# Performance work log

Hardware: AMD Instinct MI355X
Metric: run time of the kernel (lower is better)

## Reference

```python
import jax, jax.numpy as jnp
import numpy as np

DIM = 4096; H = 32; D = 128; EPS = 1e-5
BLOCK = 16
BD = 8; MAXB = 64                    # decode seqs, blocks per decode seq
PB = 2; PSEQ = 1024; TP = PB * PSEQ  # prefill: 2 seqs x 1024 tokens
TOK = TP + BD
NBLOCKS = BD * MAXB + TP // BLOCK    # 640
NEG = -1e30


def setup_inputs() -> dict:
    key = jax.random.key(0)
    ks = jax.random.split(key, 10)
    std = 0.02
    x = jax.random.normal(ks[0], (TOK, DIM), jnp.float32)
    key_heap = jax.random.normal(ks[1], (NBLOCKS, BLOCK, H, D), jnp.float32)
    val_heap = jax.random.normal(ks[2], (NBLOCKS, BLOCK, H, D), jnp.float32)
    # decode seq i owns blocks [i*MAXB, (i+1)*MAXB); context_len includes the new token
    ctx = jax.random.randint(ks[3], (BD,), 256, MAXB * BLOCK + 1).astype(jnp.int32)
    block_table = (jnp.arange(BD)[:, None] * MAXB + jnp.arange(MAXB)[None, :]).astype(jnp.int32)
    prefill_slots = BD * MAXB * BLOCK + jnp.arange(TP)      # prefill fills blocks after decode region
    decode_slots = jnp.arange(BD) * MAXB * BLOCK + (ctx - 1)  # newest-token slot per decode seq
    slot_mapping = jnp.concatenate([prefill_slots, decode_slots]).astype(jnp.int32)
    cu = (jnp.arange(PB + 1) * PSEQ).astype(jnp.int32)
    return dict(
        x=x, key_heap=key_heap, val_heap=val_heap,
        slot_mapping=slot_mapping, decode_block_table=block_table,
        decode_context_lens=ctx, prefill_cu_seqlens=cu,
        num_prefill_tokens=TP, prefill_max_seqlen=PSEQ, decode_max_seq_len=MAXB * BLOCK,
        norm1_w=1.0 + std * jax.random.normal(ks[4], (DIM,), jnp.float32),
        norm2_w=1.0 + std * jax.random.normal(ks[5], (DIM,), jnp.float32),
        w_qkv_w=std * jax.random.normal(ks[6], (3 * H * D, DIM), jnp.float32),
        wo_w=std * jax.random.normal(ks[7], (DIM, H * D), jnp.float32),
        w_gate_up_w=std * jax.random.normal(ks[8], (8 * DIM, DIM), jnp.float32),
        w2_w=std * jax.random.normal(ks[9], (DIM, 4 * DIM), jnp.float32),
    )


def _rmsnorm(x, w):
    return x * jax.lax.rsqrt(jnp.mean(x * x, -1, keepdims=True) + EPS) * w


def _forward(x, key_heap, val_heap, norm1_w, norm2_w, w_qkv_w, wo_w, w_gate_up_w, w2_w,
             slot_mapping, decode_block_table, decode_context_lens, prefill_cu_seqlens,
             num_prefill_tokens):
    T = x.shape[0]
    scale = 1.0 / np.sqrt(D)
    residual = x
    # fused norm1 -> QKV projection
    qkv = (_rmsnorm(x, norm1_w) @ w_qkv_w.T).reshape(T, 3, H, D)
    q, k, v = qkv[:, 0], qkv[:, 1], qkv[:, 2]
    # paged cache write (ops.reshape_and_cache)
    nb, bs = key_heap.shape[0], key_heap.shape[1]
    key_flat = key_heap.reshape(nb * bs, H, D).at[slot_mapping].set(k)
    val_flat = val_heap.reshape(nb * bs, H, D).at[slot_mapping].set(v)
    # prefill: varlen causal self-attention (flash_attn_varlen_func)
    Tp = num_prefill_tokens
    pos = jnp.arange(Tp)
    seg = jnp.searchsorted(prefill_cu_seqlens, pos, side='right') - 1
    mask = (seg[:, None] == seg[None, :]) & (pos[:, None] >= pos[None, :])  # [Tp,Tp]
    s = jnp.einsum('ihd,jhd->hij', q[:Tp], k[:Tp]) * scale
    attn_p = jnp.einsum('hij,jhd->ihd',
                        jax.nn.softmax(jnp.where(mask[None], s, NEG), -1), v[:Tp])
    # decode: paged attention over cached KV (ops.paged_attention_v2)
    kd = key_flat.reshape(nb, bs, H, D)[decode_block_table].reshape(BD, -1, H, D)
    vd = val_flat.reshape(nb, bs, H, D)[decode_block_table].reshape(BD, -1, H, D)
    L = kd.shape[1]
    sd = jnp.einsum('bhd,blhd->bhl', q[Tp:], kd) * scale
    dmask = jnp.arange(L)[None, :] < decode_context_lens[:, None]
    attn_d = jnp.einsum('bhl,blhd->bhd',
                        jax.nn.softmax(jnp.where(dmask[:, None, :], sd, NEG), -1), vd)
    attn = jnp.concatenate([attn_p.reshape(Tp, H * D), attn_d.reshape(BD, H * D)], 0)
    # MLP: wo + residual, norm2, SwiGLU, down-proj, residual
    h = attn @ wo_w.T + residual
    residual = h
    gu = _rmsnorm(h, norm2_w) @ w_gate_up_w.T
    g, u = jnp.split(gu, 2, -1)
    return (jax.nn.silu(g) * u) @ w2_w.T + residual


def reference(x, key_heap, val_heap, slot_mapping, decode_block_table, decode_context_lens,
              prefill_cu_seqlens, num_prefill_tokens, prefill_max_seqlen, decode_max_seq_len,
              norm1_w, norm2_w, w_qkv_w, wo_w, w_gate_up_w, w2_w):
    del prefill_max_seqlen, decode_max_seq_len  # kernel scheduling hints only
    return _forward(x, key_heap, val_heap, norm1_w, norm2_w, w_qkv_w, wo_w, w_gate_up_w, w2_w,
                    slot_mapping, decode_block_table, decode_context_lens, prefill_cu_seqlens,
                    num_prefill_tokens)
```

## Files before the change

### kernel.cpp

```cpp
#include <hip/hip_runtime.h>
#include <hip/hip_bf16.h>
#include <stdint.h>

#define DIMC   4096
#define HC     32
#define DC     128
#define TPC    2048
#define TOKC   2056
#define BDC    8
#define MAXBC  64
#define PSEQC  1024
#define QKVN   12288
#define FFNC   16384
#define PSCALE 0.08838834764831843f

typedef __attribute__((ext_vector_type(8))) short short8;
typedef __attribute__((ext_vector_type(4))) float f32x4;
typedef __attribute__((ext_vector_type(4))) unsigned short u16x4;
typedef __attribute__((ext_vector_type(8))) unsigned short u16x8;

__device__ inline unsigned short f2bf(float f) {
  union { float f; unsigned u; } v; v.f = f;
  unsigned r = v.u + 0x7FFFu + ((v.u >> 16) & 1u);
  return (unsigned short)(r >> 16);
}
__device__ inline float bf2f(unsigned short u) {
  union { unsigned u; float f; } v; v.u = ((unsigned)u) << 16;
  return v.f;
}
__device__ inline f32x4 mfma16(short8 a, short8 b, f32x4 c) {
  return __builtin_amdgcn_mfma_f32_16x16x32_bf16(a, b, c, 0, 0, 0);
}
__device__ inline void gload16(const void* g, void* l) {
  __builtin_amdgcn_global_load_lds(
      (const __attribute__((address_space(1))) void*)g,
      (__attribute__((address_space(3))) void*)l, 16, 0, 0);
}

__global__ __launch_bounds__(256) void cvt_w(
    const float* __restrict__ in, unsigned short* __restrict__ out, long n8)
{
  long i = (long)blockIdx.x * 256 + threadIdx.x;
  const long stride = (long)gridDim.x * 256;
  for (; i < n8; i += stride) {
    f32x4 a = ((const f32x4*)in)[2 * i];
    f32x4 b = ((const f32x4*)in)[2 * i + 1];
    u16x8 o;
#pragma unroll
    for (int j = 0; j < 4; ++j) { o[j] = f2bf(a[j]); o[j + 4] = f2bf(b[j]); }
    ((u16x8*)out)[i] = o;
  }
}

__global__ __launch_bounds__(256) void rmsnorm_k(
    const float* __restrict__ x, const float* __restrict__ w,
    unsigned short* __restrict__ out)
{
  const int row = blockIdx.x;
  const int tid = threadIdx.x;
  const f32x4* xr = (const f32x4*)(x + (size_t)row * DIMC);
  f32x4 v[4];
  float ss = 0.f;
#pragma unroll
  for (int i = 0; i < 4; ++i) {
    v[i] = xr[i * 256 + tid];
    ss += v[i][0]*v[i][0] + v[i][1]*v[i][1] + v[i][2]*v[i][2] + v[i][3]*v[i][3];
  }
  for (int off = 32; off; off >>= 1) ss += __shfl_xor(ss, off);
  __shared__ float sred[4];
  if ((tid & 63) == 0) sred[tid >> 6] = ss;
  __syncthreads();
  const float rms = rsqrtf((sred[0]+sred[1]+sred[2]+sred[3]) * (1.f/DIMC) + 1e-5f);
  const f32x4* wr = (const f32x4*)w;
#pragma unroll
  for (int i = 0; i < 4; ++i) {
    f32x4 wv = wr[i * 256 + tid];
    u16x4 o;
#pragma unroll
    for (int j = 0; j < 4; ++j) o[j] = f2bf(v[i][j] * rms * wv[j]);
    *(u16x4*)(out + (size_t)row * DIMC + (size_t)(i * 256 + tid) * 4) = o;
  }
}

template<int MODE, int SK>
__global__ __launch_bounds__(512, 2) void gemm8p(
    const unsigned short* __restrict__ A, const unsigned short* __restrict__ Bh,
    float* __restrict__ Cf, unsigned short* __restrict__ Cb,
    const float* __restrict__ Res, int M, int N, int K)
{
  __shared__ char ldsc[131072];
  const int tid = threadIdx.x;
  const int lane = tid & 63, wid = tid >> 6;
  const int wr = wid >> 2, wc = wid & 3;
  const int lhi = lane >> 4, llo = lane & 15;

  const int nM = (M + 255) >> 8;
  const int nN = N >> 8;
  const int nwg = gridDim.x, orig = blockIdx.x;
  const int qq = nwg >> 3, rr = nwg & 7;
  const int xcd = orig & 7, lid = orig >> 3;
  const int wgid = (xcd < rr ? xcd*(qq+1) : rr*(qq+1) + (xcd-rr)*qq) + lid;
  const int tiles = nM * nN;
  const int ks = wgid / tiles;
  const int tile = wgid % tiles;
  const int bm = (tile % nM) << 8;
  const int bn = (tile / nM) << 8;
  const int kLen = K / SK;
  const int k0 = ks * kLen;
  const int NT = kLen >> 6;

  const unsigned short* src[2][2][2];
#pragma unroll
  for (int i = 0; i < 2; ++i) {
    int s = i * 512 + tid;
    int row = s >> 3;
    int chunk = (s & 7) ^ (row & 7);
#pragma unroll
    for (int h = 0; h < 2; ++h) {
      int ga = bm + h * 128 + row; ga = ga < M ? ga : M - 1;
      src[0][h][i] = A  + (size_t)ga * K + k0 + chunk * 8;
      src[1][h][i] = Bh + (size_t)(bn + h * 128 + row) * K + k0 + chunk * 8;
    }
  }

#define STG(U, OP, H) do { \
    int bb_ = (((U) & 1) << 16) + ((OP) << 15) + ((H) << 14) + (wid << 10); \
    gload16(src[OP][H][0] + ((size_t)(U) << 6), ldsc + bb_); \
    gload16(src[OP][H][1] + ((size_t)(U) << 6), ldsc + bb_ + 8192); \
  } while (0)

#define LDA(PB, HA) do { _Pragma("unroll") for (int m_ = 0; m_ < 4; ++m_) { \
    int row_ = wr*64 + m_*16 + llo; \
    int rb_ = (PB) + ((HA) << 14) + row_*128; int sx_ = (row_ & 7) << 4; \
    ar[m_][0] = *(const short8*)(ldsc + rb_ + ((lhi*16) ^ sx_)); \
    ar[m_][1] = *(const short8*)(ldsc + rb_ + ((64 + lhi*16) ^ sx_)); } } while (0)

#define LDB(PB, HB, DST) do { _Pragma("unroll") for (int n_ = 0; n_ < 2; ++n_) { \
    int row_ = wc*32 + n_*16 + llo; \
    int rb_ = (PB) + 32768 + ((HB) << 14) + row_*128; int sx_ = (row_ & 7) << 4; \
    DST[n_][0] = *(const short8*)(ldsc + rb_ + ((lhi*16) ^ sx_)); \
    DST[n_][1] = *(const short8*)(ldsc + rb_ + ((64 + lhi*16) ^ sx_)); } } while (0)

#define MM(QA, QB, B_) do { __builtin_amdgcn_s_setprio(1); \
    _Pragma("unroll") for (int m_ = 0; m_ < 4; ++m_) \
    _Pragma("unroll") for (int n_ = 0; n_ < 2; ++n_) { \
      acc[QA][QB][m_][n_] = mfma16(ar[m_][0], B_[n_][0], acc[QA][QB][m_][n_]); \
      acc[QA][QB][m_][n_] = mfma16(ar[m_][1], B_[n_][1], acc[QA][QB][m_][n_]); } \
    __builtin_amdgcn_s_setprio(0); } while (0)

#define FEN __builtin_amdgcn_sched_barrier(0)
#define BAR __builtin_amdgcn_s_barrier()
#define VMB(N) do { FEN; asm volatile("s_waitcnt vmcnt(" #N ")" ::: "memory"); \
    BAR; FEN; } while (0)

  f32x4 acc[2][2][4][2] = {};
  short8 ar[4][2], b0[2][2], b1[2][2];

  STG(0, 0, 0); STG(0, 1, 0); STG(0, 1, 1); STG(0, 0, 1);
  STG(1, 0, 0); STG(1, 1, 0); STG(1, 1, 1);
  VMB(6);
  LDA(0, 0); LDB(0, 0, b0);

  for (int t = 0; t < NT - 2; ++t) {
    const int pb = (t & 1) << 16, pbn = ((t + 1) & 1) << 16;
    LDB(pb, 1, b1);
    STG(t + 1, 0, 1);
    MM(0, 0, b0);
    BAR;
    STG(t + 2, 0, 0);
    MM(0, 1, b1);
    LDA(pb, 1);
    BAR;
    STG(t + 2, 1, 0);
    MM(1, 1, b1);
    VMB(8);
    STG(t + 2, 1, 1);
    MM(1, 0, b0);
    LDA(pbn, 0);
    LDB(pbn, 0, b0);
    VMB(6);
  }
  {
    const int pb = ((NT - 2) & 1) << 16, pbn = ((NT - 1) & 1) << 16;
    LDB(pb, 1, b1);
    STG(NT - 1, 0, 1);
    MM(0, 0, b0);
    BAR;
    MM(0, 1, b1);
    LDA(pb, 1);
    BAR;
    MM(1, 1, b1);
    VMB(4);
    MM(1, 0, b0);
    LDA(pbn, 0);
    LDB(pbn, 0, b0);
    VMB(0);
  }
  {
    const int pb = ((NT - 1) & 1) << 16;
    LDB(pb, 1, b1);
    MM(0, 0, b0);
    MM(0, 1, b1);
    LDA(pb, 1);
    MM(1, 1, b1);
    MM(1, 0, b0);
  }

  float* Pf = (MODE == 3) ? (Cf + (size_t)ks * M * N) : Cf;
#pragma unroll
  for (int qa = 0; qa < 2; ++qa)
#pragma unroll
  for (int m_ = 0; m_ < 4; ++m_)
#pragma unroll
  for (int j = 0; j < 4; ++j) {
    int row = bm + qa*128 + wr*64 + m_*16 + lhi*4 + j;
    if (row < M) {
#pragma unroll
      for (int qb = 0; qb < 2; ++qb)
#pragma unroll
      for (int n_ = 0; n_ < 2; ++n_) {
        int col = bn + qb*128 + wc*32 + n_*16 + llo;
        float v = acc[qa][qb][m_][n_][j];
        if (MODE == 1) { v += Res[(size_t)row*N + col]; Pf[(size_t)row*N + col] = v; }
        else if (MODE == 3) { Pf[(size_t)row*N + col] = v; }
        else Cb[(size_t)row*N + col] = f2bf(v);
      }
    }
  }
#undef STG
#undef LDA
#undef LDB
#undef MM
#undef FEN
#undef BAR
#undef VMB
}

__global__ __launch_bounds__(256) void redk(
    const float* __restrict__ p, const float* __restrict__ res,
    float* __restrict__ out, long n4)
{
  long i = (long)blockIdx.x * 256 + threadIdx.x;
  if (i >= n4) return;
  const f32x4* p4 = (const f32x4*)p;
  f32x4 v = p4[i] + p4[i + n4] + p4[i + 2*n4] + p4[i + 3*n4]
          + ((const f32x4*)res)[i];
  ((f32x4*)out)[i] = v;
}

template<int MODE, int BF16B>
__global__ __launch_bounds__(256) void gemm_bt(
    const unsigned short* __restrict__ A, const float* __restrict__ Bf,
    const unsigned short* __restrict__ Bh,
    float* __restrict__ Cf, unsigned short* __restrict__ Cb,
    const float* __restrict__ Res, int M, int N, int K)
{
  __shared__ unsigned short la[128 * 64];
  __shared__ unsigned short lb[128 * 64];
  const int tid = threadIdx.x;
  const int lane = tid & 63, wid = tid >> 6;
  const int wr = wid >> 1, wc = wid & 1;
  const int lhi = lane >> 4, llo = lane & 15;

  const int nM = (M + 127) >> 7;
  const int nwg = gridDim.x;
  const int orig = blockIdx.x;
  const int qq = nwg >> 3, rr = nwg & 7;
  const int xcd = orig & 7, lid = orig >> 3;
  const int wgid = (xcd < rr ? xcd * (qq + 1) : rr * (qq + 1) + (xcd - rr) * qq) + lid;
  const int bm = (wgid % nM) * 128;
  const int bn = (wgid / nM) * 128;

  const unsigned short* aSrc[4];
  const unsigned short* bSrcH[4];
  char* aDst[4];
  char* bDst[4];
#pragma unroll
  for (int p = 0; p < 4; ++p) {
    int slot = p * 256 + tid;
    int row = slot >> 3;
    int chunk = (slot & 7) ^ (row & 7);
    int gr = bm + row; gr = gr < M ? gr : M - 1;
    aSrc[p] = A + (size_t)gr * K + chunk * 8;
    aDst[p] = (char*)la + p * 4096 + wid * 1024;
    if (BF16B) {
      bSrcH[p] = Bh + (size_t)(bn + row) * K + chunk * 8;
      bDst[p] = (char*)lb + p * 4096 + wid * 1024;
    }
  }

  f32x4 acc[4][4] = {};

  for (int k0 = 0; k0 < K; k0 += 64) {
#pragma unroll
    for (int p = 0; p < 4; ++p) gload16(aSrc[p] + k0, aDst[p]);
    if (BF16B) {
#pragma unroll
      for (int p = 0; p < 4; ++p) gload16(bSrcH[p] + k0, bDst[p]);
    } else {
#pragma unroll
      for (int p = 0; p < 4; ++p) {
        int idx = p * 256 + tid;
        int row = idx >> 3, c8 = (idx & 7) << 3;
        const float* srcf = Bf + (size_t)(bn + row) * K + k0 + c8;
        f32x4 v0 = *(const f32x4*)srcf;
        f32x4 v1 = *(const f32x4*)(srcf + 4);
        short8 bv;
#pragma unroll
        for (int i = 0; i < 4; ++i) { bv[i] = (short)f2bf(v0[i]); bv[i+4] = (short)f2bf(v1[i]); }
        int byt = (row << 7) + (c8 << 1);
        byt ^= (row & 7) << 4;
        *(short8*)((char*)lb + byt) = bv;
      }
    }
    __syncthreads();
#pragma unroll
    for (int kk = 0; kk < 64; kk += 32) {
      short8 af[4], bfr[4];
#pragma unroll
      for (int m = 0; m < 4; ++m) {
        int row = wr * 64 + m * 16 + llo;
        int byt = (row << 7) + ((kk + lhi * 8) << 1);
        byt ^= (row & 7) << 4;
        af[m] = *(const short8*)((const char*)la + byt);
      }
#pragma unroll
      for (int n = 0; n < 4; ++n) {
        int row = wc * 64 + n * 16 + llo;
        int byt = (row << 7) + ((kk + lhi * 8) << 1);
        byt ^= (row & 7) << 4;
        bfr[n] = *(const short8*)((const char*)lb + byt);
      }
#pragma unroll
      for (int m = 0; m < 4; ++m)
#pragma unroll
        for (int n = 0; n < 4; ++n)
          acc[m][n] = mfma16(af[m], bfr[n], acc[m][n]);
    }
    __syncthreads();
  }

#pragma unroll
  for (int m = 0; m < 4; ++m) {
#pragma unroll
    for (int j = 0; j < 4; ++j) {
      int row = bm + wr * 64 + m * 16 + lhi * 4 + j;
      if (row < M) {
#pragma unroll
        for (int n = 0; n < 4; ++n) {
          int col = bn + wc * 64 + n * 16 + llo;
          float v = acc[m][n][j];
          if (MODE == 1) {
            v += Res[(size_t)row * N + col];
            Cf[(size_t)row * N + col] = v;
          } else {
            Cb[(size_t)row * N + col] = f2bf(v);
          }
        }
      }
    }
  }
}

__global__ __launch_bounds__(512) void prefill_attn(
    const unsigned short* __restrict__ qkv, unsigned short* __restrict__ attnb)
{
  const int h = blockIdx.x, qtb = blockIdx.y, s = blockIdx.z;
  const int seq0 = s * PSEQC;
  const int q0 = qtb * 128;
  const int tid = threadIdx.x;
  const int lane = tid & 63, w = tid >> 6;
  const int lhi = lane >> 4, llo = lane & 15;
  const int qw = q0 + w * 16;

  __shared__ unsigned short lk[64 * 128];
  __shared__ unsigned short lvt[128 * 72];
  __shared__ unsigned short lp[8][16 * 72];

  short8 qf[4];
  {
    const unsigned short* qrow =
        qkv + (size_t)(seq0 + qw + llo) * QKVN + h * DC;
#pragma unroll
    for (int kk = 0; kk < 4; ++kk)
      qf[kk] = *(const short8*)(qrow + kk * 32 + lhi * 8);
  }

  float m_r[4], l_r[4];
#pragma unroll
  for (int r = 0; r < 4; ++r) { m_r[r] = -1e30f; l_r[r] = 0.f; }
  f32x4 oacc[8] = {};

  const int ntiles = 2 * qtb + 2;
  for (int t = 0; t < ntiles; ++t) {
    const int j0 = t * 64;
#pragma unroll
    for (int p = 0; p < 2; ++p) {
      int idx = p * 512 + tid;
      int row = idx >> 4, cs = idx & 15;
      int cg = cs ^ (row & 7);
      gload16(qkv + (size_t)(seq0 + j0 + row) * QKVN + DIMC + h * DC + cg * 8,
              (char*)lk + p * 8192 + w * 1024);
    }
    {
      int jp = tid >> 4;
      int c8 = (tid & 15) << 3;
      int j = jp * 2;
      const unsigned short* vrow =
          qkv + (size_t)(seq0 + j0 + j) * QKVN + 2 * DIMC + h * DC + c8;
      short8 v0 = *(const short8*)vrow;
      short8 v1 = *(const short8*)(vrow + QKVN);
#pragma unroll
      for (int i = 0; i < 8; ++i) {
        int d = c8 + i;
        int jj = j ^ (((d >> 3) & 7) << 3);
        unsigned pack = (unsigned)(unsigned short)v0[i]
                      | ((unsigned)(unsigned short)v1[i] << 16);
        *(unsigned*)(lvt + d * 72 + jj) = pack;
      }
    }
    asm volatile("s_waitcnt vmcnt(0)" ::: "memory");
    __syncthreads();

    const bool active = (j0 <= qw + 15);
    if (active) {
      f32x4 sfr[4] = {};
#pragma unroll
      for (int n = 0; n < 4; ++n) {
        int row = n * 16 + llo;
#pragma unroll
        for (int kk = 0; kk < 4; ++kk) {
          int col = (kk * 32 + lhi * 8) ^ ((row & 7) << 3);
          short8 kf = *(const short8*)(lk + row * 128 + col);
          sfr[n] = mfma16(qf[kk], kf, sfr[n]);
        }
      }

      const bool diag = (j0 + 63 > qw);
      const int qbase = qw + lhi * 4;
      float pv[4][4];
#pragma unroll
      for (int r = 0; r < 4; ++r) {
        float mx = -1e30f;
#pragma unroll
        for (int n = 0; n < 4; ++n) {
          float sv = sfr[n][r] * PSCALE;
          if (diag && (j0 + n * 16 + llo > qbase + r)) sv = -1e30f;
          pv[n][r] = sv;
          mx = fmaxf(mx, sv);
        }
        for (int off = 8; off; off >>= 1) mx = fmaxf(mx, __shfl_xor(mx, off));
        float mnew = fmaxf(m_r[r], mx);
        float alpha = __expf(m_r[r] - mnew);
        m_r[r] = mnew;
        float rs = 0.f;
#pragma unroll
        for (int n = 0; n < 4; ++n) {
          float p = __expf(pv[n][r] - mnew);
          pv[n][r] = p;
          rs += p;
        }
        for (int off = 8; off; off >>= 1) rs += __shfl_xor(rs, off);
        l_r[r] = l_r[r] * alpha + rs;
#pragma unroll
        for (int f = 0; f < 8; ++f) oacc[f][r] *= alpha;
      }

      unsigned short* lpw = lp[w];
#pragma unroll
      for (int r = 0; r < 4; ++r)
#pragma unroll
        for (int n = 0; n < 4; ++n)
          lpw[(lhi * 4 + r) * 72 + n * 16 + llo] = f2bf(pv[n][r]);

#pragma unroll
      for (int kk = 0; kk < 2; ++kk) {
        short8 pf = *(const short8*)(lpw + llo * 72 + kk * 32 + lhi * 8);
#pragma unroll
        for (int f = 0; f < 8; ++f) {
          int d = f * 16 + llo;
          int jb = kk * 32 + lhi * 8;
          int jj = jb ^ (((d >> 3) & 7) << 3);
          short8 vf = *(const short8*)(lvt + d * 72 + jj);
          oacc[f] = mfma16(pf, vf, oacc[f]);
        }
      }
    }
    __syncthreads();
  }

#pragma unroll
  for (int r = 0; r < 4; ++r) {
    int row = seq0 + qw + lhi * 4 + r;
    float inv = 1.f / l_r[r];
#pragma unroll
    for (int f = 0; f < 8; ++f)
      attnb[(size_t)row * DIMC + h * DC + f * 16 + llo] = f2bf(oacc[f][r] * inv);
  }
}

__global__ __launch_bounds__(256) void decode_attn(
    const unsigned short* __restrict__ qkv,
    const float* __restrict__ kheap, const float* __restrict__ vheap,
    const int* __restrict__ btab, const int* __restrict__ ctxl,
    unsigned short* __restrict__ attnb)
{
  const int h = blockIdx.x, b = blockIdx.y;
  const int ctx = ctxl[b];
  const int tq = TPC + b;
  const int tid = threadIdx.x;
  __shared__ float sq[DC];
  __shared__ float sp[1024];
  __shared__ float sred[4];
  __shared__ float obuf[DC];

  const unsigned short* qrow = qkv + (size_t)tq * QKVN + h * DC;
  if (tid < DC) sq[tid] = bf2f(qrow[tid]);
  __syncthreads();

  float lmax = -1e30f;
#pragma unroll
  for (int i = 0; i < 4; ++i) {
    int l = i * 256 + tid;
    float sv = -1e30f;
    if (l < ctx) {
      float accd = 0.f;
      if (l == ctx - 1) {
        const unsigned short* kn = qkv + (size_t)tq * QKVN + DIMC + h * DC;
        for (int d = 0; d < DC; ++d) accd += sq[d] * bf2f(kn[d]);
      } else {
        int blk = btab[b * MAXBC + (l >> 4)];
        const float* kp = kheap + (((size_t)blk * 16 + (l & 15)) * HC + h) * DC;
#pragma unroll
        for (int d = 0; d < DC; d += 4) {
          f32x4 kv = *(const f32x4*)(kp + d);
          accd += sq[d] * kv[0] + sq[d+1] * kv[1] + sq[d+2] * kv[2] + sq[d+3] * kv[3];
        }
      }
      sv = accd * PSCALE;
    }
    sp[l] = sv;
    lmax = fmaxf(lmax, sv);
  }
  for (int off = 32; off; off >>= 1) lmax = fmaxf(lmax, __shfl_xor(lmax, off));
  if ((tid & 63) == 0) sred[tid >> 6] = lmax;
  __syncthreads();
  const float m = fmaxf(fmaxf(sred[0], sred[1]), fmaxf(sred[2], sred[3]));
  __syncthreads();

  float lsum = 0.f;
#pragma unroll
  for (int i = 0; i < 4; ++i) {
    int l = i * 256 + tid;
    float p = __expf(sp[l] - m);
    sp[l] = p;
    lsum += p;
  }
  for (int off = 32; off; off >>= 1) lsum += __shfl_xor(lsum, off);
  if ((tid & 63) == 0) sred[tid >> 6] = lsum;
  __syncthreads();
  const float denom = sred[0] + sred[1] + sred[2] + sred[3];

  const int d = tid & 127, half = tid >> 7;
  float o = 0.f;
  for (int l = half; l < ctx; l += 2) {
    float p = sp[l];
    float v;
    if (l == ctx - 1) {
      v = bf2f(qkv[(size_t)tq * QKVN + 2 * DIMC + h * DC + d]);
    } else {
      int blk = btab[b * MAXBC + (l >> 4)];
      v = vheap[(((size_t)blk * 16 + (l & 15)) * HC + h) * DC + d];
    }
    o += p * v;
  }
  if (half) obuf[d] = o;
  __syncthreads();
  if (!half)
    attnb[(size_t)tq * DIMC + h * DC + d] = f2bf((o + obuf[d]) / denom);
}

__global__ __launch_bounds__(256) void silu_mul(
    const unsigned short* __restrict__ gu, unsigned short* __restrict__ act)
{
  size_t chunk = (size_t)blockIdx.x * 256 + threadIdx.x;
  size_t row = chunk >> 11;
  int c = (int)(chunk & 2047) << 3;
  const unsigned short* g = gu + row * (2 * FFNC) + c;
  u16x8 gv = *(const u16x8*)g;
  u16x8 uv = *(const u16x8*)(g + FFNC);
  u16x8 o;
#pragma unroll
  for (int i = 0; i < 8; ++i) {
    float gf = bf2f(gv[i]);
    float uf = bf2f(uv[i]);
    float sf = gf / (1.f + __expf(-gf));
    o[i] = f2bf(sf * uf);
  }
  *(u16x8*)(act + row * FFNC + c) = o;
}

extern "C" void kernel_launch(void* const* d_in, const int* in_sizes, int n_in,
                              void* d_out, int out_size, void* d_ws, size_t ws_size,
                              hipStream_t stream) {
  const float* x     = (const float*)d_in[0];
  const float* kheap = (const float*)d_in[1];
  const float* vheap = (const float*)d_in[2];
  const int*   btab  = (const int*)d_in[4];
  const int*   ctxl  = (const int*)d_in[5];
  const float* n1w   = (const float*)d_in[10];
  const float* n2w   = (const float*)d_in[11];
  const float* wqkv  = (const float*)d_in[12];
  const float* wo    = (const float*)d_in[13];
  const float* wgu   = (const float*)d_in[14];
  const float* w2    = (const float*)d_in[15];
  float* out = (float*)d_out;

  char* ws = (char*)d_ws;
  unsigned short* xn   = (unsigned short*)(ws);
  unsigned short* qkvb = (unsigned short*)(ws + 16842752);
  unsigned short* actb = qkvb;
  unsigned short* attn = (unsigned short*)(ws + 16842752 + 67371008);
  float*          hbuf = (float*)(ws + 16842752 + 67371008 + 16842752);
  unsigned short* gub  = (unsigned short*)(ws + 16842752 + 67371008 + 16842752 + 33685504);

  const size_t wbase = 269484032;
  const bool bw = ws_size >= wbase + 536870912ull;
  unsigned short* wqkv_h = (unsigned short*)(ws + wbase);
  unsigned short* wo_h   = (unsigned short*)(ws + wbase + 100663296);
  unsigned short* wgu_h  = (unsigned short*)(ws + wbase + 100663296 + 33554432);
  unsigned short* w2_h   = (unsigned short*)(ws + wbase + 100663296 + 33554432 + 268435456);
  const size_t pko = wbase + 536870912ull;
  const bool sk4 = bw && (ws_size >= pko + 134742016ull);
  float* pbuf = (float*)(ws + pko);

  if (bw) {
    cvt_w<<<2048, 256, 0, stream>>>(wqkv, wqkv_h, (long)QKVN * DIMC / 8);
    cvt_w<<<2048, 256, 0, stream>>>(wo,   wo_h,   (long)DIMC * DIMC / 8);
    cvt_w<<<2048, 256, 0, stream>>>(wgu,  wgu_h,  (long)2 * FFNC * DIMC / 8);
    cvt_w<<<2048, 256, 0, stream>>>(w2,   w2_h,   (long)DIMC * FFNC / 8);
  }

  const int nM8 = 9;
  const int nM4 = 17;

  rmsnorm_k<<<TOKC, 256, 0, stream>>>(x, n1w, xn);
  if (bw) gemm8p<2,1><<<nM8 * (QKVN/256), 512, 0, stream>>>(xn, wqkv_h, nullptr, qkvb, nullptr, TOKC, QKVN, DIMC);
  else    gemm_bt<2,0><<<nM4 * (QKVN/128), 256, 0, stream>>>(xn, wqkv, nullptr, nullptr, qkvb, nullptr, TOKC, QKVN, DIMC);
  prefill_attn<<<dim3(HC, PSEQC / 128, 2), 512, 0, stream>>>(qkvb, attn);
  decode_attn<<<dim3(HC, BDC), 256, 0, stream>>>(qkvb, kheap, vheap, btab, ctxl, attn);
  if (bw) gemm_bt<1,1><<<nM4 * (DIMC/128), 256, 0, stream>>>(attn, nullptr, wo_h, hbuf, nullptr, x, TOKC, DIMC, DIMC);
  else    gemm_bt<1,0><<<nM4 * (DIMC/128), 256, 0, stream>>>(attn, wo, nullptr, hbuf, nullptr, x, TOKC, DIMC, DIMC);
  rmsnorm_k<<<TOKC, 256, 0, stream>>>(hbuf, n2w, xn);
  if (bw) gemm8p<2,1><<<nM8 * (2*FFNC/256), 512, 0, stream>>>(xn, wgu_h, nullptr, gub, nullptr, TOKC, 2*FFNC, DIMC);
  else    gemm_bt<2,0><<<nM4 * (2*FFNC/128), 256, 0, stream>>>(xn, wgu, nullptr, nullptr, gub, nullptr, TOKC, 2*FFNC, DIMC);
  silu_mul<<<(TOKC * (FFNC / 8)) / 256, 256, 0, stream>>>(gub, actb);
  if (sk4) {
    gemm8p<3,4><<<nM8 * (DIMC/256) * 4, 512, 0, stream>>>(actb, w2_h, pbuf, nullptr, nullptr, TOKC, DIMC, FFNC);
    redk<<<(TOKC * DIMC / 4 + 255) / 256, 256, 0, stream>>>(pbuf, hbuf, out, (long)TOKC * DIMC / 4);
  } else if (bw) {
    gemm8p<1,1><<<nM8 * (DIMC/256), 512, 0, stream>>>(actb, w2_h, out, nullptr, hbuf, TOKC, DIMC, FFNC);
  } else {
    gemm_bt<1,0><<<nM4 * (DIMC/128), 256, 0, stream>>>(actb, w2, nullptr, out, nullptr, hbuf, TOKC, DIMC, FFNC);
  }
}
```

Measured before the change: 1.901 ms.

## Overlap weight conversions with GEMMs and fuse SiLU-mul into gate-up epilogue

Weight fp32-to-bf16 conversion for wo, gate-up and w2 moves into extra workgroups appended to the QKV and gate-up GEMM launches (grid 1280), so conversion runs alongside tile compute instead of as separate serial kernels. The gate-up weight is row-permuted during conversion so gate and up columns interleave per 16-column group. This lets a new epilogue mode apply SiLU(g)*u directly and write the activation, removing the separate silu_mul kernel and the gub round-trip. The cost is extra kernel arguments, converter blocks contending for bandwidth with GEMM tiles, and reliance on a specific permutation layout.

```diff
diff --git a/kernel.cpp b/kernel.cpp
--- a/kernel.cpp
+++ b/kernel.cpp
@@ -86,7 +86,9 @@
 __global__ __launch_bounds__(512, 2) void gemm8p(
     const unsigned short* __restrict__ A, const unsigned short* __restrict__ Bh,
     float* __restrict__ Cf, unsigned short* __restrict__ Cb,
-    const float* __restrict__ Res, int M, int N, int K)
+    const float* __restrict__ Res, int M, int N, int K,
+    const float* cv1In, unsigned short* cv1Out, long cv1N8, int cv1Perm,
+    const float* cv2In, unsigned short* cv2Out, long cv2N8)
 {
   __shared__ char ldsc[131072];
   const int tid = threadIdx.x;
@@ -100,9 +102,45 @@
   const int qq = nwg >> 3, rr = nwg & 7;
   const int xcd = orig & 7, lid = orig >> 3;
   const int wgid = (xcd < rr ? xcd*(qq+1) : rr*(qq+1) + (xcd-rr)*qq) + lid;
-  const int tiles = nM * nN;
-  const int ks = wgid / tiles;
-  const int tile = wgid % tiles;
+  const int tilesTotal = nM * nN * SK;
+
+  if (wgid >= tilesTotal) {
+    const long cid = wgid - tilesTotal;
+    const long CVB = (long)nwg - tilesTotal;
+    const long tot = cv1N8 + cv2N8;
+    for (long i = cid * 512 + tid; i < tot; i += CVB * 512) {
+      if (i < cv1N8) {
+        long e8 = i;
+        long srcE8;
+        if (cv1Perm) {
+          long r2 = e8 >> 9, c8 = e8 & 511;
+          long b = r2 >> 5, off = r2 & 31;
+          long srcr = (off < 16) ? (b * 16 + off) : (16384 + b * 16 + (off & 15));
+          srcE8 = srcr * 512 + c8;
+        } else {
+          srcE8 = e8;
+        }
+        f32x4 a = ((const f32x4*)cv1In)[2 * srcE8];
+        f32x4 b2 = ((const f32x4*)cv1In)[2 * srcE8 + 1];
+        u16x8 o;
+#pragma unroll
+        for (int j = 0; j < 4; ++j) { o[j] = f2bf(a[j]); o[j + 4] = f2bf(b2[j]); }
+        ((u16x8*)cv1Out)[e8] = o;
+      } else {
+        long e8 = i - cv1N8;
+        f32x4 a = ((const f32x4*)cv2In)[2 * e8];
+        f32x4 b2 = ((const f32x4*)cv2In)[2 * e8 + 1];
+        u16x8 o;
+#pragma unroll
+        for (int j = 0; j < 4; ++j) { o[j] = f2bf(a[j]); o[j + 4] = f2bf(b2[j]); }
+        ((u16x8*)cv2Out)[e8] = o;
+      }
+    }
+    return;
+  }
+
+  const int ks = wgid / (nM * nN);
+  const int tile = wgid % (nM * nN);
   const int bm = (tile % nM) << 8;
   const int bn = (tile / nM) << 8;
   const int kLen = K / SK;
@@ -215,15 +253,26 @@
   for (int j = 0; j < 4; ++j) {
     int row = bm + qa*128 + wr*64 + m_*16 + lhi*4 + j;
     if (row < M) {
-#pragma unroll
-      for (int qb = 0; qb < 2; ++qb)
-#pragma unroll
-      for (int n_ = 0; n_ < 2; ++n_) {
-        int col = bn + qb*128 + wc*32 + n_*16 + llo;
-        float v = acc[qa][qb][m_][n_][j];
-        if (MODE == 1) { v += Res[(size_t)row*N + col]; Pf[(size_t)row*N + col] = v; }
-        else if (MODE == 3) { Pf[(size_t)row*N + col] = v; }
-        else Cb[(size_t)row*N + col] = f2bf(v);
+      if (MODE == 4) {
+#pragma unroll
+        for (int qb = 0; qb < 2; ++qb) {
+          int base = bn + qb*128 + wc*32;
+          float g = acc[qa][qb][m_][0][j];
+          float u = acc[qa][qb][m_][1][j];
+          float sv = g / (1.f + __expf(-g)) * u;
+          Cb[(size_t)row * (N >> 1) + (base >> 1) + llo] = f2bf(sv);
+        }
+      } else {
+#pragma unroll
+        for (int qb = 0; qb < 2; ++qb)
+#pragma unroll
+        for (int n_ = 0; n_ < 2; ++n_) {
+          int col = bn + qb*128 + wc*32 + n_*16 + llo;
+          float v = acc[qa][qb][m_][n_][j];
+          if (MODE == 1) { v += Res[(size_t)row*N + col]; Pf[(size_t)row*N + col] = v; }
+          else if (MODE == 3) { Pf[(size_t)row*N + col] = v; }
+          else Cb[(size_t)row*N + col] = f2bf(v);
+        }
       }
     }
   }
@@ -634,33 +683,44 @@
   const bool sk4 = bw && (ws_size >= pko + 134742016ull);
   float* pbuf = (float*)(ws + pko);
 
+  const int nM8 = 9;
+  const int nM4 = 17;
+  const long wguN8 = (long)2 * FFNC * DIMC / 8;
+  const long woN8  = (long)DIMC * DIMC / 8;
+  const long w2N8  = (long)DIMC * FFNC / 8;
+
+  rmsnorm_k<<<TOKC, 256, 0, stream>>>(x, n1w, xn);
+
   if (bw) {
     cvt_w<<<2048, 256, 0, stream>>>(wqkv, wqkv_h, (long)QKVN * DIMC / 8);
-    cvt_w<<<2048, 256, 0, stream>>>(wo,   wo_h,   (long)DIMC * DIMC / 8);
-    cvt_w<<<2048, 256, 0, stream>>>(wgu,  wgu_h,  (long)2 * FFNC * DIMC / 8);
-    cvt_w<<<2048, 256, 0, stream>>>(w2,   w2_h,   (long)DIMC * FFNC / 8);
-  }
-
-  const int nM8 = 9;
-  const int nM4 = 17;
-
-  rmsnorm_k<<<TOKC, 256, 0, stream>>>(x, n1w, xn);
-  if (bw) gemm8p<2,1><<<nM8 * (QKVN/256), 512, 0, stream>>>(xn, wqkv_h, nullptr, qkvb, nullptr, TOKC, QKVN, DIMC);
-  else    gemm_bt<2,0><<<nM4 * (QKVN/128), 256, 0, stream>>>(xn, wqkv, nullptr, nullptr, qkvb, nullptr, TOKC, QKVN, DIMC);
-  prefill_attn<<<dim3(HC, PSEQC / 128, 2), 512, 0, stream>>>(qkvb, attn);
-  decode_attn<<<dim3(HC, BDC), 256, 0, stream>>>(qkvb, kheap, vheap, btab, ctxl, attn);
-  if (bw) gemm_bt<1,1><<<nM4 * (DIMC/128), 256, 0, stream>>>(attn, nullptr, wo_h, hbuf, nullptr, x, TOKC, DIMC, DIMC);
-  else    gemm_bt<1,0><<<nM4 * (DIMC/128), 256, 0, stream>>>(attn, wo, nullptr, hbuf, nullptr, x, TOKC, DIMC, DIMC);
-  rmsnorm_k<<<TOKC, 256, 0, stream>>>(hbuf, n2w, xn);
-  if (bw) gemm8p<2,1><<<nM8 * (2*FFNC/256), 512, 0, stream>>>(xn, wgu_h, nullptr, gub, nullptr, TOKC, 2*FFNC, DIMC);
-  else    gemm_bt<2,0><<<nM4 * (2*FFNC/128), 256, 0, stream>>>(xn, wgu, nullptr, nullptr, gub, nullptr, TOKC, 2*FFNC, DIMC);
-  silu_mul<<<(TOKC * (FFNC / 8)) / 256, 256, 0, stream>>>(gub, actb);
-  if (sk4) {
-    gemm8p<3,4><<<nM8 * (DIMC/256) * 4, 512, 0, stream>>>(actb, w2_h, pbuf, nullptr, nullptr, TOKC, DIMC, FFNC);
-    redk<<<(TOKC * DIMC / 4 + 255) / 256, 256, 0, stream>>>(pbuf, hbuf, out, (long)TOKC * DIMC / 4);
-  } else if (bw) {
-    gemm8p<1,1><<<nM8 * (DIMC/256), 512, 0, stream>>>(actb, w2_h, out, nullptr, hbuf, TOKC, DIMC, FFNC);
+    gemm8p<2,1><<<1280, 512, 0, stream>>>(
+        xn, wqkv_h, nullptr, qkvb, nullptr, TOKC, QKVN, DIMC,
+        wgu, wgu_h, wguN8, 1, wo, wo_h, woN8);
+    prefill_attn<<<dim3(HC, PSEQC / 128, 2), 512, 0, stream>>>(qkvb, attn);
+    decode_attn<<<dim3(HC, BDC), 256, 0, stream>>>(qkvb, kheap, vheap, btab, ctxl, attn);
+    gemm_bt<1,1><<<nM4 * (DIMC/128), 256, 0, stream>>>(attn, nullptr, wo_h, hbuf, nullptr, x, TOKC, DIMC, DIMC);
+    rmsnorm_k<<<TOKC, 256, 0, stream>>>(hbuf, n2w, xn);
+    gemm8p<4,1><<<1280, 512, 0, stream>>>(
+        xn, wgu_h, nullptr, actb, nullptr, TOKC, 2*FFNC, DIMC,
+        w2, w2_h, w2N8, 0, nullptr, nullptr, 0);
+    if (sk4) {
+      gemm8p<3,4><<<nM8 * (DIMC/256) * 4, 512, 0, stream>>>(
+          actb, w2_h, pbuf, nullptr, nullptr, TOKC, DIMC, FFNC,
+          nullptr, nullptr, 0, 0, nullptr, nullptr, 0);
+      redk<<<(TOKC * DIMC / 4 + 255) / 256, 256, 0, stream>>>(pbuf, hbuf, out, (long)TOKC * DIMC / 4);
+    } else {
+      gemm8p<1,1><<<nM8 * (DIMC/256), 512, 0, stream>>>(
+          actb, w2_h, out, nullptr, hbuf, TOKC, DIMC, FFNC,
+          nullptr, nullptr, 0, 0, nullptr, nullptr, 0);
+    }
   } else {
+    gemm_bt<2,0><<<nM4 * (QKVN/128), 256, 0, stream>>>(xn, wqkv, nullptr, nullptr, qkvb, nullptr, TOKC, QKVN, DIMC);
+    prefill_attn<<<dim3(HC, PSEQC / 128, 2), 512, 0, stream>>>(qkvb, attn);
+    decode_attn<<<dim3(HC, BDC), 256, 0, stream>>>(qkvb, kheap, vheap, btab, ctxl, attn);
+    gemm_bt<1,0><<<nM4 * (DIMC/128), 256, 0, stream>>>(attn, wo, nullptr, hbuf, nullptr, x, TOKC, DIMC, DIMC);
+    rmsnorm_k<<<TOKC, 256, 0, stream>>>(hbuf, n2w, xn);
+    gemm_bt<2,0><<<nM4 * (2*FFNC/128), 256, 0, stream>>>(xn, wgu, nullptr, nullptr, gub, nullptr, TOKC, 2*FFNC, DIMC);
+    silu_mul<<<(TOKC * (FFNC / 8)) / 256, 256, 0, stream>>>(gub, actb);
     gemm_bt<1,0><<<nM4 * (DIMC/128), 256, 0, stream>>>(actb, w2, nullptr, out, nullptr, hbuf, TOKC, DIMC, FFNC);
   }
 }
```

Result: slower. 1.970 ms (+3.6%).

## Fuse SiLU-gate multiply into gate/up GEMM epilogue via interleaved weight rows

Applied to the files above, without the earlier changes.

Permutes the gate/up weight rows during bf16 conversion so that each 16-column output group of gate sits next to the matching up group. A new GEMM epilogue mode then computes silu(g)*u in registers and writes the half-width activation directly. This removes the bf16 round trip of the full gate/up output and the separate silu_mul kernel. The cost is a strided gather in the weight conversion and narrower scattered bf16 stores in the epilogue.

```diff
diff --git a/kernel.cpp b/kernel.cpp
--- a/kernel.cpp
+++ b/kernel.cpp
@@ -48,6 +48,25 @@
     u16x8 o;
 #pragma unroll
     for (int j = 0; j < 4; ++j) { o[j] = f2bf(a[j]); o[j + 4] = f2bf(b[j]); }
+    ((u16x8*)out)[i] = o;
+  }
+}
+
+__global__ __launch_bounds__(256) void cvt_wgu_perm(
+    const float* __restrict__ in, unsigned short* __restrict__ out, long n8)
+{
+  long i = (long)blockIdx.x * 256 + threadIdx.x;
+  const long stride = (long)gridDim.x * 256;
+  for (; i < n8; i += stride) {
+    long r2 = i >> 9, c8 = i & 511;
+    long b = r2 >> 5, off = r2 & 31;
+    long srcr = (off < 16) ? (b * 16 + off) : (16384 + b * 16 + (off & 15));
+    long s8 = srcr * 512 + c8;
+    f32x4 a = ((const f32x4*)in)[2 * s8];
+    f32x4 b2 = ((const f32x4*)in)[2 * s8 + 1];
+    u16x8 o;
+#pragma unroll
+    for (int j = 0; j < 4; ++j) { o[j] = f2bf(a[j]); o[j + 4] = f2bf(b2[j]); }
     ((u16x8*)out)[i] = o;
   }
 }
@@ -215,15 +234,26 @@
   for (int j = 0; j < 4; ++j) {
     int row = bm + qa*128 + wr*64 + m_*16 + lhi*4 + j;
     if (row < M) {
-#pragma unroll
-      for (int qb = 0; qb < 2; ++qb)
-#pragma unroll
-      for (int n_ = 0; n_ < 2; ++n_) {
-        int col = bn + qb*128 + wc*32 + n_*16 + llo;
-        float v = acc[qa][qb][m_][n_][j];
-        if (MODE == 1) { v += Res[(size_t)row*N + col]; Pf[(size_t)row*N + col] = v; }
-        else if (MODE == 3) { Pf[(size_t)row*N + col] = v; }
-        else Cb[(size_t)row*N + col] = f2bf(v);
+      if (MODE == 4) {
+#pragma unroll
+        for (int qb = 0; qb < 2; ++qb) {
+          int base = bn + qb*128 + wc*32;
+          float g = acc[qa][qb][m_][0][j];
+          float u = acc[qa][qb][m_][1][j];
+          float sv = g / (1.f + __expf(-g)) * u;
+          Cb[(size_t)row * (N >> 1) + (base >> 1) + llo] = f2bf(sv);
+        }
+      } else {
+#pragma unroll
+        for (int qb = 0; qb < 2; ++qb)
+#pragma unroll
+        for (int n_ = 0; n_ < 2; ++n_) {
+          int col = bn + qb*128 + wc*32 + n_*16 + llo;
+          float v = acc[qa][qb][m_][n_][j];
+          if (MODE == 1) { v += Res[(size_t)row*N + col]; Pf[(size_t)row*N + col] = v; }
+          else if (MODE == 3) { Pf[(size_t)row*N + col] = v; }
+          else Cb[(size_t)row*N + col] = f2bf(v);
+        }
       }
     }
   }
@@ -634,33 +664,39 @@
   const bool sk4 = bw && (ws_size >= pko + 134742016ull);
   float* pbuf = (float*)(ws + pko);
 
+  const int nM8 = 9;
+  const int nM4 = 17;
+
   if (bw) {
     cvt_w<<<2048, 256, 0, stream>>>(wqkv, wqkv_h, (long)QKVN * DIMC / 8);
     cvt_w<<<2048, 256, 0, stream>>>(wo,   wo_h,   (long)DIMC * DIMC / 8);
-    cvt_w<<<2048, 256, 0, stream>>>(wgu,  wgu_h,  (long)2 * FFNC * DIMC / 8);
-    cvt_w<<<2048, 256, 0, stream>>>(w2,   w2_h,   (long)DIMC * FFNC / 8);
-  }
-
-  const int nM8 = 9;
-  const int nM4 = 17;
+    cvt_wgu_perm<<<2048, 256, 0, stream>>>(wgu, wgu_h, (long)2 * FFNC * DIMC / 8);
+    cvt_w<<<2048, 256, 0, stream>>>(w2,   w2_h,  (long)DIMC * FFNC / 8);
+  }
 
   rmsnorm_k<<<TOKC, 256, 0, stream>>>(x, n1w, xn);
-  if (bw) gemm8p<2,1><<<nM8 * (QKVN/256), 512, 0, stream>>>(xn, wqkv_h, nullptr, qkvb, nullptr, TOKC, QKVN, DIMC);
-  else    gemm_bt<2,0><<<nM4 * (QKVN/128), 256, 0, stream>>>(xn, wqkv, nullptr, nullptr, qkvb, nullptr, TOKC, QKVN, DIMC);
-  prefill_attn<<<dim3(HC, PSEQC / 128, 2), 512, 0, stream>>>(qkvb, attn);
-  decode_attn<<<dim3(HC, BDC), 256, 0, stream>>>(qkvb, kheap, vheap, btab, ctxl, attn);
-  if (bw) gemm_bt<1,1><<<nM4 * (DIMC/128), 256, 0, stream>>>(attn, nullptr, wo_h, hbuf, nullptr, x, TOKC, DIMC, DIMC);
-  else    gemm_bt<1,0><<<nM4 * (DIMC/128), 256, 0, stream>>>(attn, wo, nullptr, hbuf, nullptr, x, TOKC, DIMC, DIMC);
-  rmsnorm_k<<<TOKC, 256, 0, stream>>>(hbuf, n2w, xn);
-  if (bw) gemm8p<2,1><<<nM8 * (2*FFNC/256), 512, 0, stream>>>(xn, wgu_h, nullptr, gub, nullptr, TOKC, 2*FFNC, DIMC);
-  else    gemm_bt<2,0><<<nM4 * (2*FFNC/128), 256, 0, stream>>>(xn, wgu, nullptr, nullptr, gub, nullptr, TOKC, 2*FFNC, DIMC);
-  silu_mul<<<(TOKC * (FFNC / 8)) / 256, 256, 0, stream>>>(gub, actb);
-  if (sk4) {
-    gemm8p<3,4><<<nM8 * (DIMC/256) * 4, 512, 0, stream>>>(actb, w2_h, pbuf, nullptr, nullptr, TOKC, DIMC, FFNC);
-    redk<<<(TOKC * DIMC / 4 + 255) / 256, 256, 0, stream>>>(pbuf, hbuf, out, (long)TOKC * DIMC / 4);
-  } else if (bw) {
-    gemm8p<1,1><<<nM8 * (DIMC/256), 512, 0, stream>>>(actb, w2_h, out, nullptr, hbuf, TOKC, DIMC, FFNC);
+
+  if (bw) {
+    gemm8p<2,1><<<nM8 * (QKVN/256), 512, 0, stream>>>(xn, wqkv_h, nullptr, qkvb, nullptr, TOKC, QKVN, DIMC);
+    prefill_attn<<<dim3(HC, PSEQC / 128, 2), 512, 0, stream>>>(qkvb, attn);
+    decode_attn<<<dim3(HC, BDC), 256, 0, stream>>>(qkvb, kheap, vheap, btab, ctxl, attn);
+    gemm_bt<1,1><<<nM4 * (DIMC/128), 256, 0, stream>>>(attn, nullptr, wo_h, hbuf, nullptr, x, TOKC, DIMC, DIMC);
+    rmsnorm_k<<<TOKC, 256, 0, stream>>>(hbuf, n2w, xn);
+    gemm8p<4,1><<<nM8 * (2*FFNC/256), 512, 0, stream>>>(xn, wgu_h, nullptr, actb, nullptr, TOKC, 2*FFNC, DIMC);
+    if (sk4) {
+      gemm8p<3,4><<<nM8 * (DIMC/256) * 4, 512, 0, stream>>>(actb, w2_h, pbuf, nullptr, nullptr, TOKC, DIMC, FFNC);
+      redk<<<(TOKC * DIMC / 4 + 255) / 256, 256, 0, stream>>>(pbuf, hbuf, out, (long)TOKC * DIMC / 4);
+    } else {
+      gemm8p<1,1><<<nM8 * (DIMC/256), 512, 0, stream>>>(actb, w2_h, out, nullptr, hbuf, TOKC, DIMC, FFNC);
+    }
   } else {
+    gemm_bt<2,0><<<nM4 * (QKVN/128), 256, 0, stream>>>(xn, wqkv, nullptr, nullptr, qkvb, nullptr, TOKC, QKVN, DIMC);
+    prefill_attn<<<dim3(HC, PSEQC / 128, 2), 512, 0, stream>>>(qkvb, attn);
+    decode_attn<<<dim3(HC, BDC), 256, 0, stream>>>(qkvb, kheap, vheap, btab, ctxl, attn);
+    gemm_bt<1,0><<<nM4 * (DIMC/128), 256, 0, stream>>>(attn, wo, nullptr, hbuf, nullptr, x, TOKC, DIMC, DIMC);
+    rmsnorm_k<<<TOKC, 256, 0, stream>>>(hbuf, n2w, xn);
+    gemm_bt<2,0><<<nM4 * (2*FFNC/128), 256, 0, stream>>>(xn, wgu, nullptr, nullptr, gub, nullptr, TOKC, 2*FFNC, DIMC);
+    silu_mul<<<(TOKC * (FFNC / 8)) / 256, 256, 0, stream>>>(gub, actb);
     gemm_bt<1,0><<<nM4 * (DIMC/128), 256, 0, stream>>>(actb, w2, nullptr, out, nullptr, hbuf, TOKC, DIMC, FFNC);
   }
 }
```

After: 1.858 ms. 1.02x faster.
